# Kernel tuning notes

Measured on AMD Instinct MI355X. Metric: run time of the kernel, lower is better.

The kernel has to match this reference:

```python
import jax, jax.numpy as jnp
import numpy as np
from jax import lax

H = 2  # hidden_size == input_size == 2 (hardcoded in the module)


def _gru_cell(x, h, w_ih, w_hh, b_ih):
    # PyTorch GRUCell math with bias_hh frozen to zero.
    gi = x @ w_ih.T + b_ih          # [B, 3H]
    gh = h @ w_hh.T                 # [B, 3H], b_hh == 0
    i_r, i_z, i_n = gi[:, :H], gi[:, H:2 * H], gi[:, 2 * H:]
    h_r, h_z, h_n = gh[:, :H], gh[:, H:2 * H], gh[:, 2 * H:]
    r = jax.nn.sigmoid(i_r + h_r)
    z = jax.nn.sigmoid(i_z + h_z)
    n = jnp.tanh(i_n + r * h_n)
    return (1.0 - z) * n + z * h


def setup_inputs() -> dict:
    key = jax.random.key(0)
    B, T, G = 2097152, 8, 2  # batch, unroll_for, num_gru
    k1, k2, k3, k4, k5 = jax.random.split(key, 5)
    s = 1.0 / np.sqrt(H)  # PyTorch GRUCell init scale
    return {
        "inputs": jax.random.normal(k1, (B, H), jnp.float32),
        "labels": jax.random.normal(k2, (B, T, H), jnp.float32),
        "w_ih": jax.random.uniform(k3, (G, 3 * H, H), jnp.float32, -s, s),
        "w_hh": jax.random.uniform(k4, (G, 3 * H, H), jnp.float32, -s, s),
        "b_ih": jax.random.uniform(k5, (G, 3 * H), jnp.float32, -s, s),
    }


def reference(inputs, labels, w_ih, w_hh, b_ih):
    G = w_ih.shape[0]
    T = labels.shape[1]

    def step(carry, _):
        hs, out = carry  # hs: [G, B, H], out: [B, H]
        new_hs = []
        for i in range(G):  # small fixed stack of structurally distinct cells
            h = _gru_cell(out, hs[i], w_ih[i], w_hh[i], b_ih[i])
            new_hs.append(h)
            out = h
        return (jnp.stack(new_hs), out), out

    hs0 = jnp.zeros((G,) + inputs.shape, inputs.dtype)
    _, rets = lax.scan(step, (hs0, inputs), None, length=T)  # rets: [T, B, H]
    ret = jnp.transpose(rets, (1, 0, 2))  # [B, T, H]
    loss = jnp.mean(jnp.square(ret - labels))
    return ret, loss
```

## Files before the change

kernel.cpp:

```cpp
#include <hip/hip_runtime.h>


typedef float v2f __attribute__((ext_vector_type(2)));
typedef float v4f __attribute__((ext_vector_type(4)));

__device__ __forceinline__ v2f v2(float a, float b) { v2f r; r.x = a; r.y = b; return r; }
__device__ __forceinline__ v2f vbc(float a) { return v2(a, a); }
__device__ __forceinline__ v2f vswap(v2f a) { return __builtin_shufflevector(a, a, 1, 0); }
__device__ __forceinline__ v2f vfma(v2f a, v2f b, v2f c) { return __builtin_elementwise_fma(a, b, c); }

__device__ __forceinline__ v2f sig_from_scaled(v2f y) {
    v2f e;
    e.x = __builtin_amdgcn_exp2f(y.x);
    e.y = __builtin_amdgcn_exp2f(y.y);
    const v2f d = e + vbc(1.0f);
    v2f q;
    q.x = __builtin_amdgcn_rcpf(d.x);
    q.y = __builtin_amdgcn_rcpf(d.y);
    return q;
}

__device__ __forceinline__ v2f gru_cell(v2f o, v2f h,
    const v2f wihA[3], const v2f wihB[3],
    const v2f whhA[3], const v2f whhB[3], const v2f bpk[3])
{
    const v2f os = vswap(o);
    const v2f hs = vswap(h);
    v2f rin = vfma(wihA[0], o,
              vfma(wihB[0], os,
              vfma(whhA[0], h,
              vfma(whhB[0], hs, bpk[0]))));
    v2f zin = vfma(wihA[1], o,
              vfma(wihB[1], os,
              vfma(whhA[1], h,
              vfma(whhB[1], hs, bpk[1]))));
    v2f gin = vfma(wihA[2], o, vfma(wihB[2], os, bpk[2]));
    v2f ghn = vfma(whhA[2], h, whhB[2] * hs);

    const v2f r = sig_from_scaled(rin);
    const v2f z = sig_from_scaled(zin);
    const v2f q = sig_from_scaled(vfma(r, ghn, gin));
    const v2f n = vfma(vbc(2.0f), q, vbc(-1.0f));
    return vfma(z, h - n, n);
}

__global__ __launch_bounds__(256) void gru_fused(
    const float* __restrict__ inputs,
    const float* __restrict__ labels,
    const float* __restrict__ w_ih,
    const float* __restrict__ w_hh,
    const float* __restrict__ b_ih,
    float* __restrict__ out,
    float* __restrict__ partials)
{
    __shared__ float lds[256 * 17];
    const int tid = threadIdx.x;
    const int e0  = blockIdx.x * 512 + tid;
    const int e1  = e0 + 256;

    const float2 xA = reinterpret_cast<const float2*>(inputs)[e0];
    const float2 xB = reinterpret_cast<const float2*>(inputs)[e1];

    v2f wihA[2][3], wihB[2][3], whhA[2][3], whhB[2][3], bpk[2][3];
#pragma unroll
    for (int g = 0; g < 2; ++g) {
#pragma unroll
        for (int p = 0; p < 3; ++p) {
            const float hf = (p < 2) ? -1.442695040888963f : -2.885390081777927f;
            const int r0 = g * 12 + (2 * p) * 2;
            const int r1 = g * 12 + (2 * p + 1) * 2;
            wihA[g][p] = v2(w_ih[r0 + 0] * hf, w_ih[r1 + 1] * hf);
            wihB[g][p] = v2(w_ih[r0 + 1] * hf, w_ih[r1 + 0] * hf);
            whhA[g][p] = v2(w_hh[r0 + 0] * hf, w_hh[r1 + 1] * hf);
            whhB[g][p] = v2(w_hh[r0 + 1] * hf, w_hh[r1 + 0] * hf);
            bpk[g][p]  = v2(b_ih[g * 6 + 2 * p] * hf, b_ih[g * 6 + 2 * p + 1] * hf);
        }
    }

    v2f hA[2] = { vbc(0.0f), vbc(0.0f) }, hB[2] = { vbc(0.0f), vbc(0.0f) };
    v2f oA = v2(xA.x, xA.y), oB = v2(xB.x, xB.y);
    v2f resA[8], resB[8];

#pragma unroll
    for (int t = 0; t < 8; ++t) {
#pragma unroll
        for (int g = 0; g < 2; ++g) {
            hA[g] = gru_cell(oA, hA[g], wihA[g], wihB[g], whhA[g], whhB[g], bpk[g]);
            oA = hA[g];
            hB[g] = gru_cell(oB, hB[g], wihA[g], wihB[g], whhA[g], whhB[g], bpk[g]);
            oB = hB[g];
        }
        resA[t] = oA;
        resB[t] = oB;
    }

    const v4f* labd = reinterpret_cast<const v4f*>(labels)
                    + (size_t)blockIdx.x * 2048 + tid;
    v4f labA[4], labB[4];
#pragma unroll
    for (int c = 0; c < 4; ++c) labA[c] = labd[c * 256];
#pragma unroll
    for (int c = 0; c < 4; ++c) labB[c] = labd[1024 + c * 256];

    v4f* outd = reinterpret_cast<v4f*>(out) + (size_t)blockIdx.x * 2048 + tid;
    float lsum = 0.0f;

#pragma unroll
    for (int q = 0; q < 8; ++q) {
        lds[tid * 17 + 2 * q + 0] = resA[q].x;
        lds[tid * 17 + 2 * q + 1] = resA[q].y;
    }
    __syncthreads();
#pragma unroll
    for (int c = 0; c < 4; ++c) {
        const int f4   = c * 256 + tid;
        const int base = (f4 >> 2) * 17 + (f4 & 3) * 4;
        v4f ov;
        ov.x = lds[base + 0]; ov.y = lds[base + 1];
        ov.z = lds[base + 2]; ov.w = lds[base + 3];
        __builtin_nontemporal_store(ov, &outd[c * 256]);
        const v4f d = ov - labA[c];
        lsum += (d.x * d.x + d.y * d.y) + (d.z * d.z + d.w * d.w);
    }
    __syncthreads();

#pragma unroll
    for (int q = 0; q < 8; ++q) {
        lds[tid * 17 + 2 * q + 0] = resB[q].x;
        lds[tid * 17 + 2 * q + 1] = resB[q].y;
    }
    __syncthreads();
#pragma unroll
    for (int c = 0; c < 4; ++c) {
        const int f4   = c * 256 + tid;
        const int base = (f4 >> 2) * 17 + (f4 & 3) * 4;
        v4f ov;
        ov.x = lds[base + 0]; ov.y = lds[base + 1];
        ov.z = lds[base + 2]; ov.w = lds[base + 3];
        __builtin_nontemporal_store(ov, &outd[1024 + c * 256]);
        const v4f d = ov - labB[c];
        lsum += (d.x * d.x + d.y * d.y) + (d.z * d.z + d.w * d.w);
    }

#pragma unroll
    for (int off = 32; off > 0; off >>= 1)
        lsum += __shfl_down(lsum, off, 64);
    __shared__ float wsum[4];
    const int lane = tid & 63;
    const int wid  = tid >> 6;
    if (lane == 0) wsum[wid] = lsum;
    __syncthreads();
    if (tid == 0)
        partials[blockIdx.x] = (wsum[0] + wsum[1]) + (wsum[2] + wsum[3]);
}

__global__ __launch_bounds__(1024) void gru_loss_reduce(
    const v4f* __restrict__ partials4, int n4,
    float* __restrict__ loss_out, double inv_n)
{
    float s = 0.0f;
    for (int i = threadIdx.x; i < n4; i += 1024) {
        const v4f p = partials4[i];
        s += (p.x + p.y) + (p.z + p.w);
    }
#pragma unroll
    for (int off = 32; off > 0; off >>= 1)
        s += __shfl_down(s, off, 64);
    __shared__ float wsum[16];
    const int lane = threadIdx.x & 63;
    const int wid  = threadIdx.x >> 6;
    if (lane == 0) wsum[wid] = s;
    __syncthreads();
    if (threadIdx.x == 0) {
        double tot = 0.0;
#pragma unroll
        for (int i = 0; i < 16; ++i) tot += (double)wsum[i];
        *loss_out = (float)(tot * inv_n);
    }
}

extern "C" void kernel_launch(void* const* d_in, const int* in_sizes, int n_in,
                              void* d_out, int out_size, void* d_ws, size_t ws_size,
                              hipStream_t stream) {
    const float* inputs = (const float*)d_in[0];
    const float* labels = (const float*)d_in[1];
    const float* w_ih   = (const float*)d_in[2];
    const float* w_hh   = (const float*)d_in[3];
    const float* b_ih   = (const float*)d_in[4];
    float* out      = (float*)d_out;
    float* partials = (float*)d_ws;

    const int B    = in_sizes[0] / 2;
    const int NE   = B * 16;
    const int grid = B / 512;

    gru_fused<<<grid, 256, 0, stream>>>(inputs, labels, w_ih, w_hh, b_ih,
                                        out, partials);
    gru_loss_reduce<<<1, 1024, 0, stream>>>((const v4f*)partials, grid / 4,
                                            out + NE, 1.0 / (double)NE);
}
```

Before: 59.18 us.

## Prefetch labels into LDS asynchronously and serialize the two GRU chains

```diff
diff --git a/kernel.cpp b/kernel.cpp
--- a/kernel.cpp
+++ b/kernel.cpp
@@ -9,7 +9,7 @@
 __device__ __forceinline__ v2f vswap(v2f a) { return __builtin_shufflevector(a, a, 1, 0); }
 __device__ __forceinline__ v2f vfma(v2f a, v2f b, v2f c) { return __builtin_elementwise_fma(a, b, c); }
 
-__device__ __forceinline__ v2f sig_from_scaled(v2f y) {
+__device__ __forceinline__ v2f sig2(v2f y) {
     v2f e;
     e.x = __builtin_amdgcn_exp2f(y.x);
     e.y = __builtin_amdgcn_exp2f(y.y);
@@ -37,11 +37,17 @@
     v2f gin = vfma(wihA[2], o, vfma(wihB[2], os, bpk[2]));
     v2f ghn = vfma(whhA[2], h, whhB[2] * hs);
 
-    const v2f r = sig_from_scaled(rin);
-    const v2f z = sig_from_scaled(zin);
-    const v2f q = sig_from_scaled(vfma(r, ghn, gin));
+    const v2f r = sig2(rin);
+    const v2f z = sig2(zin);
+    const v2f q = sig2(vfma(r, ghn, gin));
     const v2f n = vfma(vbc(2.0f), q, vbc(-1.0f));
     return vfma(z, h - n, n);
+}
+
+__device__ __forceinline__ void gload_lds16(const v4f* g, v4f* l) {
+    __builtin_amdgcn_global_load_lds(
+        (const __attribute__((address_space(1))) void*)g,
+        (__attribute__((address_space(3))) void*)l, 16, 0, 0);
 }
 
 __global__ __launch_bounds__(256) void gru_fused(
@@ -53,13 +59,24 @@
     float* __restrict__ out,
     float* __restrict__ partials)
 {
-    __shared__ float lds[256 * 17];
+    __shared__ v4f   labA_lds[1024];
+    __shared__ v4f   labB_lds[1024];
+    __shared__ float ldsT[256 * 17];
     const int tid = threadIdx.x;
+    const int wv  = tid >> 6;
     const int e0  = blockIdx.x * 512 + tid;
-    const int e1  = e0 + 256;
 
     const float2 xA = reinterpret_cast<const float2*>(inputs)[e0];
-    const float2 xB = reinterpret_cast<const float2*>(inputs)[e1];
+    const float2 xB = reinterpret_cast<const float2*>(inputs)[e0 + 256];
+    const v4f* labd = reinterpret_cast<const v4f*>(labels)
+                    + (size_t)blockIdx.x * 2048 + tid;
+#pragma unroll
+    for (int c = 0; c < 4; ++c)
+        gload_lds16(labd + c * 256, &labA_lds[c * 256 + wv * 64]);
+#pragma unroll
+    for (int c = 0; c < 4; ++c)
+        gload_lds16(labd + 1024 + c * 256, &labB_lds[c * 256 + wv * 64]);
+    __builtin_amdgcn_sched_barrier(0);
 
     v2f wihA[2][3], wihB[2][3], whhA[2][3], whhB[2][3], bpk[2][3];
 #pragma unroll
@@ -77,38 +94,27 @@
         }
     }
 
-    v2f hA[2] = { vbc(0.0f), vbc(0.0f) }, hB[2] = { vbc(0.0f), vbc(0.0f) };
-    v2f oA = v2(xA.x, xA.y), oB = v2(xB.x, xB.y);
-    v2f resA[8], resB[8];
-
-#pragma unroll
-    for (int t = 0; t < 8; ++t) {
-#pragma unroll
-        for (int g = 0; g < 2; ++g) {
-            hA[g] = gru_cell(oA, hA[g], wihA[g], wihB[g], whhA[g], whhB[g], bpk[g]);
-            oA = hA[g];
-            hB[g] = gru_cell(oB, hB[g], wihA[g], wihB[g], whhA[g], whhB[g], bpk[g]);
-            oB = hB[g];
-        }
-        resA[t] = oA;
-        resB[t] = oB;
-    }
-
-    const v4f* labd = reinterpret_cast<const v4f*>(labels)
-                    + (size_t)blockIdx.x * 2048 + tid;
-    v4f labA[4], labB[4];
-#pragma unroll
-    for (int c = 0; c < 4; ++c) labA[c] = labd[c * 256];
-#pragma unroll
-    for (int c = 0; c < 4; ++c) labB[c] = labd[1024 + c * 256];
-
     v4f* outd = reinterpret_cast<v4f*>(out) + (size_t)blockIdx.x * 2048 + tid;
     float lsum = 0.0f;
 
-#pragma unroll
-    for (int q = 0; q < 8; ++q) {
-        lds[tid * 17 + 2 * q + 0] = resA[q].x;
-        lds[tid * 17 + 2 * q + 1] = resA[q].y;
+    {
+        v2f h[2] = { vbc(0.0f), vbc(0.0f) };
+        v2f o = v2(xA.x, xA.y);
+        v2f res[8];
+#pragma unroll
+        for (int t = 0; t < 8; ++t) {
+#pragma unroll
+            for (int g = 0; g < 2; ++g) {
+                h[g] = gru_cell(o, h[g], wihA[g], wihB[g], whhA[g], whhB[g], bpk[g]);
+                o = h[g];
+            }
+            res[t] = o;
+        }
+#pragma unroll
+        for (int q = 0; q < 8; ++q) {
+            ldsT[tid * 17 + 2 * q + 0] = res[q].x;
+            ldsT[tid * 17 + 2 * q + 1] = res[q].y;
+        }
     }
     __syncthreads();
 #pragma unroll
@@ -116,29 +122,47 @@
         const int f4   = c * 256 + tid;
         const int base = (f4 >> 2) * 17 + (f4 & 3) * 4;
         v4f ov;
-        ov.x = lds[base + 0]; ov.y = lds[base + 1];
-        ov.z = lds[base + 2]; ov.w = lds[base + 3];
+        ov.x = ldsT[base + 0]; ov.y = ldsT[base + 1];
+        ov.z = ldsT[base + 2]; ov.w = ldsT[base + 3];
         __builtin_nontemporal_store(ov, &outd[c * 256]);
-        const v4f d = ov - labA[c];
+        const v4f d = ov - labA_lds[c * 256 + tid];
         lsum += (d.x * d.x + d.y * d.y) + (d.z * d.z + d.w * d.w);
     }
-    __syncthreads();
-
-#pragma unroll
-    for (int q = 0; q < 8; ++q) {
-        lds[tid * 17 + 2 * q + 0] = resB[q].x;
-        lds[tid * 17 + 2 * q + 1] = resB[q].y;
-    }
-    __syncthreads();
+    asm volatile("s_waitcnt lgkmcnt(0)" ::: "memory");
+    __builtin_amdgcn_s_barrier();
+    __builtin_amdgcn_sched_barrier(0);
+
+    {
+        v2f h[2] = { vbc(0.0f), vbc(0.0f) };
+        v2f o = v2(xB.x, xB.y);
+        v2f res[8];
+#pragma unroll
+        for (int t = 0; t < 8; ++t) {
+#pragma unroll
+            for (int g = 0; g < 2; ++g) {
+                h[g] = gru_cell(o, h[g], wihA[g], wihB[g], whhA[g], whhB[g], bpk[g]);
+                o = h[g];
+            }
+            res[t] = o;
+        }
+#pragma unroll
+        for (int q = 0; q < 8; ++q) {
+            ldsT[tid * 17 + 2 * q + 0] = res[q].x;
+            ldsT[tid * 17 + 2 * q + 1] = res[q].y;
+        }
+    }
+    asm volatile("s_waitcnt lgkmcnt(0)" ::: "memory");
+    __builtin_amdgcn_s_barrier();
+    __builtin_amdgcn_sched_barrier(0);
 #pragma unroll
     for (int c = 0; c < 4; ++c) {
         const int f4   = c * 256 + tid;
         const int base = (f4 >> 2) * 17 + (f4 & 3) * 4;
         v4f ov;
-        ov.x = lds[base + 0]; ov.y = lds[base + 1];
-        ov.z = lds[base + 2]; ov.w = lds[base + 3];
+        ov.x = ldsT[base + 0]; ov.y = ldsT[base + 1];
+        ov.z = ldsT[base + 2]; ov.w = ldsT[base + 3];
         __builtin_nontemporal_store(ov, &outd[1024 + c * 256]);
-        const v4f d = ov - labB[c];
+        const v4f d = ov - labB_lds[c * 256 + tid];
         lsum += (d.x * d.x + d.y * d.y) + (d.z * d.z + d.w * d.w);
     }
 
@@ -147,9 +171,10 @@
         lsum += __shfl_down(lsum, off, 64);
     __shared__ float wsum[4];
     const int lane = tid & 63;
-    const int wid  = tid >> 6;
-    if (lane == 0) wsum[wid] = lsum;
-    __syncthreads();
+    if (lane == 0) wsum[wv] = lsum;
+    asm volatile("s_waitcnt lgkmcnt(0)" ::: "memory");
+    __builtin_amdgcn_s_barrier();
+    __builtin_amdgcn_sched_barrier(0);
     if (tid == 0)
         partials[blockIdx.x] = (wsum[0] + wsum[1]) + (wsum[2] + wsum[3]);
 }
```

After: 59.74 us. About the same (+1.0%).

## Fuse loss reduction into main kernel with last-block atomic counter

Applied to the files above, without the earlier changes.

```diff
diff --git a/kernel.cpp b/kernel.cpp
--- a/kernel.cpp
+++ b/kernel.cpp
@@ -9,7 +9,7 @@
 __device__ __forceinline__ v2f vswap(v2f a) { return __builtin_shufflevector(a, a, 1, 0); }
 __device__ __forceinline__ v2f vfma(v2f a, v2f b, v2f c) { return __builtin_elementwise_fma(a, b, c); }
 
-__device__ __forceinline__ v2f sig_from_scaled(v2f y) {
+__device__ __forceinline__ v2f sig2(v2f y) {
     v2f e;
     e.x = __builtin_amdgcn_exp2f(y.x);
     e.y = __builtin_amdgcn_exp2f(y.y);
@@ -37,9 +37,9 @@
     v2f gin = vfma(wihA[2], o, vfma(wihB[2], os, bpk[2]));
     v2f ghn = vfma(whhA[2], h, whhB[2] * hs);
 
-    const v2f r = sig_from_scaled(rin);
-    const v2f z = sig_from_scaled(zin);
-    const v2f q = sig_from_scaled(vfma(r, ghn, gin));
+    const v2f r = sig2(rin);
+    const v2f z = sig2(zin);
+    const v2f q = sig2(vfma(r, ghn, gin));
     const v2f n = vfma(vbc(2.0f), q, vbc(-1.0f));
     return vfma(z, h - n, n);
 }
@@ -51,7 +51,9 @@
     const float* __restrict__ w_hh,
     const float* __restrict__ b_ih,
     float* __restrict__ out,
-    float* __restrict__ partials)
+    unsigned int* __restrict__ counter,
+    float* __restrict__ partials,
+    int ne, double inv_n)
 {
     __shared__ float lds[256 * 17];
     const int tid = threadIdx.x;
@@ -146,36 +148,39 @@
     for (int off = 32; off > 0; off >>= 1)
         lsum += __shfl_down(lsum, off, 64);
     __shared__ float wsum[4];
+    __shared__ int is_last;
     const int lane = tid & 63;
     const int wid  = tid >> 6;
     if (lane == 0) wsum[wid] = lsum;
     __syncthreads();
-    if (tid == 0)
-        partials[blockIdx.x] = (wsum[0] + wsum[1]) + (wsum[2] + wsum[3]);
-}
-
-__global__ __launch_bounds__(1024) void gru_loss_reduce(
-    const v4f* __restrict__ partials4, int n4,
-    float* __restrict__ loss_out, double inv_n)
-{
-    float s = 0.0f;
-    for (int i = threadIdx.x; i < n4; i += 1024) {
-        const v4f p = partials4[i];
-        s += (p.x + p.y) + (p.z + p.w);
-    }
-#pragma unroll
-    for (int off = 32; off > 0; off >>= 1)
-        s += __shfl_down(s, off, 64);
-    __shared__ float wsum[16];
-    const int lane = threadIdx.x & 63;
-    const int wid  = threadIdx.x >> 6;
-    if (lane == 0) wsum[wid] = s;
-    __syncthreads();
-    if (threadIdx.x == 0) {
-        double tot = 0.0;
-#pragma unroll
-        for (int i = 0; i < 16; ++i) tot += (double)wsum[i];
-        *loss_out = (float)(tot * inv_n);
+    if (tid == 0) {
+        const float s = (wsum[0] + wsum[1]) + (wsum[2] + wsum[3]);
+        __hip_atomic_store(&partials[blockIdx.x], s,
+                           __ATOMIC_RELAXED, __HIP_MEMORY_SCOPE_AGENT);
+        const unsigned int old =
+            __hip_atomic_fetch_add(counter, 1u,
+                                   __ATOMIC_ACQ_REL, __HIP_MEMORY_SCOPE_AGENT);
+        is_last = (old == gridDim.x - 1) ? 1 : 0;
+    }
+    __syncthreads();
+
+    if (is_last) {
+        const int nblk = gridDim.x;
+        float s = 0.0f;
+        for (int i = tid; i < nblk; i += 256)
+            s += __hip_atomic_load(&partials[i],
+                                   __ATOMIC_RELAXED, __HIP_MEMORY_SCOPE_AGENT);
+#pragma unroll
+        for (int off = 32; off > 0; off >>= 1)
+            s += __shfl_down(s, off, 64);
+        __shared__ float w2[4];
+        if (lane == 0) w2[wid] = s;
+        __syncthreads();
+        if (tid == 0) {
+            const double tot = (double)w2[0] + (double)w2[1]
+                             + (double)w2[2] + (double)w2[3];
+            out[ne] = (float)(tot * inv_n);
+        }
     }
 }
 
@@ -187,15 +192,18 @@
     const float* w_ih   = (const float*)d_in[2];
     const float* w_hh   = (const float*)d_in[3];
     const float* b_ih   = (const float*)d_in[4];
-    float* out      = (float*)d_out;
-    float* partials = (float*)d_ws;
+    float* out = (float*)d_out;
+
+    unsigned int* counter = (unsigned int*)d_ws;
+    float* partials = (float*)((char*)d_ws + 256);
 
     const int B    = in_sizes[0] / 2;
     const int NE   = B * 16;
     const int grid = B / 512;
 
+    hipMemsetAsync(d_ws, 0, 256, stream);
+
     gru_fused<<<grid, 256, 0, stream>>>(inputs, labels, w_ih, w_hh, b_ih,
-                                        out, partials);
-    gru_loss_reduce<<<1, 1024, 0, stream>>>((const v4f*)partials, grid / 4,
-                                            out + NE, 1.0 / (double)NE);
-}
+                                        out, counter, partials,
+                                        NE, 1.0 / (double)NE);
+}
```

New measurement: 202.8 us. 243% more time.
